# Performance work log

Measured on AMD Instinct MI355X. Metric: run time of the kernel, lower is better.

## Reference

```python
import jax, jax.numpy as jnp
import numpy as np

B, F0, D = 4096, 39, 16
CROSS_LAYER_SIZE = (128, 128)


def _he_uniform(key, shape):
    fan_in = int(np.prod(shape[:-1]))
    limit = np.sqrt(6.0 / fan_in)
    return jax.random.uniform(key, shape, jnp.float32, -limit, limit)


def setup_inputs() -> dict:
    key = jax.random.key(0)
    k_x, k_f0, k_f1, k_w, k_b = jax.random.split(key, 5)
    x = jax.random.normal(k_x, (B, F0, D), dtype=jnp.float32)
    # field_nums with direct=False: [39, 128//2=64, 64]
    f0 = _he_uniform(k_f0, (F0 * F0, CROSS_LAYER_SIZE[0]))          # (1521, 128)
    f1 = _he_uniform(k_f1, (F0 * (CROSS_LAYER_SIZE[0] // 2), CROSS_LAYER_SIZE[1]))  # (2496, 128)
    out_dim = CROSS_LAYER_SIZE[0] // 2 + CROSS_LAYER_SIZE[1]        # 192
    dense_w = _he_uniform(k_w, (out_dim, 1))
    dense_b = jnp.zeros((1,), dtype=jnp.float32)
    return {"x": x, "f0": f0, "f1": f1, "dense_w": dense_w, "dense_b": dense_b}


def reference(x, f0, f1, dense_w, dense_b):
    # CIN forward (direct=False, use_bias=False, use_residual=False, relu)
    # x: (B, F0, D)
    filters = [f0, f1]
    n_layers = len(CROSS_LAYER_SIZE)
    h = x  # hidden state, (B, Fk, D)
    finals = []
    for idx, L in enumerate(CROSS_LAYER_SIZE):
        Fk = h.shape[1]
        # filter f_ has shape (F0*Fk, L) with i (field of x0) major, j (field of h) minor
        Wr = filters[idx].reshape(F0, Fk, L)
        # fused outer product + conv1d (kernel width 1 == matmul over i,j):
        # z[b, m, d] = sum_{i,j} x[b,i,d] * h[b,j,d] * W[i,j,m]
        z = jnp.einsum('bid,bjd,ijm->bmd', x, h, Wr)  # (B, L, D)
        z = jax.nn.relu(z)
        if idx != n_layers - 1:
            # split along feature-map axis: first half feeds next layer,
            # second half goes to output
            h = z[:, : L // 2, :]
            finals.append(z[:, L // 2:, :])
        else:
            finals.append(z)
    result = jnp.sum(jnp.concatenate(finals, axis=1), axis=-1)  # (B, 192)
    return result @ dense_w + dense_b  # (B, 1)
```

## Files before the change

### kernel.cpp

```cpp
#include <hip/hip_runtime.h>


typedef _Float16 h2    __attribute__((ext_vector_type(2)));
typedef _Float16 f16x8 __attribute__((ext_vector_type(8)));
typedef __attribute__((ext_vector_type(16))) float f32x16;

#define XBB 1160
#define L0C 30
#define NCH 110

__device__ __constant__ int IG0[L0C] = {0,0,0,0,0, 1,1,1,1,1, 2,2,2,2, 3,3,3,3, 4,4,4, 5,5,5, 6,6, 7,7, 8, 9};
__device__ __constant__ int JG0[L0C] = {0,1,2,3,4, 0,1,2,3,4, 1,2,3,4, 1,2,3,4, 2,3,4, 2,3,4, 3,4, 3,4, 4, 4};
#define IG0T(c) ((c)<5?0:(c)<10?1:(c)<14?2:(c)<18?3:(c)<21?4:(c)<24?5:(c)<26?6:(c)<28?7:(c)<29?8:9)
#define JG0T(c) ((c)<10?((c)%5):(c)<18?(((c)-10)%4+1):(c)<24?(((c)-18)%3+2):(c)<28?(((c)-24)%2+3):4)

__global__ __launch_bounds__(256)
void CIN_repack(const float* __restrict__ f0, const float* __restrict__ f1,
                uint4* __restrict__ ws)
{
    const int tid  = blockIdx.x * 256 + threadIdx.x;
    const int n    = tid & 127;
    const int slot = tid >> 7;
    const int half = slot & 1;
    const int kh   = (slot >> 1) & 1;
    const int ch   = slot >> 2;
    float v[8];
    if (ch < L0C) {
        const int ig = IG0[ch], jg = JG0[ch];
        const int i = ig * 4 + kh * 2 + half;
#pragma unroll
        for (int t = 0; t < 8; ++t) {
            const int j = jg * 8 + t;
            float val = 0.f;
            if (i < 39 && j < 39 && j >= i) {
                val = f0[(i * 39 + j) * 128 + n];
                if (j > i) val += f0[(j * 39 + i) * 128 + n];
            }
            v[t] = val;
        }
    } else {
        const int c1 = ch - L0C;
        const int jg = c1 / 5, ig = c1 - jg * 5;
        const int j = jg * 4 + kh * 2 + half;
#pragma unroll
        for (int t = 0; t < 8; ++t) {
            const int i = ig * 8 + t;
            v[t] = (i < 39) ? f1[(i * 64 + j) * 128 + n] : 0.f;
        }
    }
    union { h2 h[4]; uint4 q; } pk;
#pragma unroll
    for (int t = 0; t < 4; ++t)
        pk.h[t] = h2{(_Float16)v[2 * t], (_Float16)v[2 * t + 1]};
    const int lane = half * 32 + (n & 31);
    const int cg   = n >> 5;
    ws[ch * 512 + kh * 256 + cg * 64 + lane] = pk.q;
}

__global__ __launch_bounds__(256, 2)
void CIN_main(const float* __restrict__ x,
              const char* __restrict__ wsB,
              const float* __restrict__ dw,
              const float* __restrict__ db,
              float* __restrict__ out)
{
    __shared__ __align__(16) _Float16 xsH[8 * XBB];
    __shared__ __align__(4)  _Float16 hsH[8][64][18];
    __shared__ float dws[192];
    __shared__ float red[4][4];

    const int tid  = threadIdx.x;
    const int w    = tid >> 6;
    const int wp   = w >> 1;
    const int wn   = w & 1;
    const int lane = tid & 63;
    const int half = lane >> 5;
    const int d    = lane & 15;
    const int bsel = (lane >> 4) & 1;
    const int col  = lane & 31;

    const char* wbase = wsB + lane * 16 + wn * 2048 + 2560;
    f16x8 Bb[2][2][2];
    auto loadBg = [&](int ch, f16x8 (&B)[2][2]) {
        const char* p0 = wbase + (size_t)ch * 8192;
        B[0][0] = *(const f16x8*)(p0 - 2560);
        B[0][1] = *(const f16x8*)(p0 - 1536);
        B[1][0] = *(const f16x8*)(p0 + 1536);
        B[1][1] = *(const f16x8*)(p0 + 2560);
    };

    loadBg(0, Bb[0]);
    loadBg(1, Bb[1]);

    const float4* xg4 = (const float4*)(x + (size_t)blockIdx.x * 8 * 624);
    for (int e4 = tid; e4 < 1248; e4 += 256) {
        float4 v = xg4[e4];
        int bb = e4 / 156, r = e4 - bb * 156;
        int i = r >> 2, d0 = (r & 3) * 4;
        _Float16* bp = xsH + bb * XBB + i;
        bp[(d0 + 0) * 72] = (_Float16)v.x; bp[(d0 + 1) * 72] = (_Float16)v.y;
        bp[(d0 + 2) * 72] = (_Float16)v.z; bp[(d0 + 3) * 72] = (_Float16)v.w;
    }
    if (tid < 128) { int bb = tid >> 4, dd = tid & 15; xsH[bb * XBB + dd * 72 + 39] = (_Float16)0.f; }
    if (tid < 192) dws[tid] = dw[tid];
    __syncthreads();

    const _Float16* xrow[2] = {
        xsH + ((wp * 2 + 0) * 2 + bsel) * XBB + d * 72,
        xsH + ((wp * 2 + 1) * 2 + bsel) * XBB + d * 72
    };

    h2 xw[2][20];
#pragma unroll
    for (int p = 0; p < 2; ++p)
#pragma unroll
        for (int w5 = 0; w5 < 5; ++w5) {
            union { f16x8 v; h2 h[4]; } u;
            u.v = *(const f16x8*)(xrow[p] + w5 * 8);
#pragma unroll
            for (int q = 0; q < 4; ++q) xw[p][w5 * 4 + q] = u.h[q];
        }

    f32x16 acc[2][2];
#pragma unroll
    for (int p = 0; p < 2; ++p)
#pragma unroll
        for (int nq = 0; nq < 2; ++nq)
#pragma unroll
            for (int r = 0; r < 16; ++r) acc[p][nq][r] = 0.f;

    h2 sp2[2][2];

#pragma unroll
    for (int c = 0; c < L0C; ++c) {
        const int ig = IG0T(c);
        const int jg = JG0T(c);
        if ((c == 0) || (IG0T(c) != IG0T(c - 1))) {
#pragma unroll
            for (int p = 0; p < 2; ++p)
#pragma unroll
                for (int kh = 0; kh < 2; ++kh) {
                    const h2 pr = xw[p][ig * 2 + kh];
                    const _Float16 vv = half ? pr.y : pr.x;
                    sp2[p][kh] = h2{vv, vv};
                }
        }
#pragma unroll
        for (int p = 0; p < 2; ++p) {
            union { h2 h[4]; f16x8 v; } a0, a1;
#pragma unroll
            for (int q = 0; q < 4; ++q) {
                a0.h[q] = sp2[p][0] * xw[p][jg * 4 + q];
                a1.h[q] = sp2[p][1] * xw[p][jg * 4 + q];
            }
            acc[p][0] = __builtin_amdgcn_mfma_f32_32x32x16_f16(a0.v, Bb[c & 1][0][0], acc[p][0], 0, 0, 0);
            acc[p][1] = __builtin_amdgcn_mfma_f32_32x32x16_f16(a0.v, Bb[c & 1][0][1], acc[p][1], 0, 0, 0);
            acc[p][0] = __builtin_amdgcn_mfma_f32_32x32x16_f16(a1.v, Bb[c & 1][1][0], acc[p][0], 0, 0, 0);
            acc[p][1] = __builtin_amdgcn_mfma_f32_32x32x16_f16(a1.v, Bb[c & 1][1][1], acc[p][1], 0, 0, 0);
        }
        loadBg(c + 2, Bb[c & 1]);
        __builtin_amdgcn_s_barrier();
    }

    float cs[4] = {0.f, 0.f, 0.f, 0.f};
    if (wn == 0) {
#pragma unroll
        for (int p = 0; p < 2; ++p)
#pragma unroll
            for (int nq = 0; nq < 2; ++nq)
#pragma unroll
                for (int r = 0; r < 16; r += 2) {
                    const int row = (r & 3) + 8 * (r >> 2) + 4 * half;
                    h2 pr = h2{(_Float16)fmaxf(acc[p][nq][r],     0.f),
                               (_Float16)fmaxf(acc[p][nq][r + 1], 0.f)};
                    *(h2*)&hsH[(wp * 2 + p) * 2 + (row >> 4)][nq * 32 + col][row & 15] = pr;
                }
    } else {
#pragma unroll
        for (int nq = 0; nq < 2; ++nq) {
            const float dwv = dws[nq * 32 + col];
#pragma unroll
            for (int p = 0; p < 2; ++p)
#pragma unroll
                for (int r = 0; r < 16; ++r) {
                    const int row = (r & 3) + 8 * (r >> 2) + 4 * half;
                    cs[p * 2 + (row >> 4)] += fmaxf(acc[p][nq][r], 0.f) * dwv;
                }
        }
    }
#pragma unroll
    for (int p = 0; p < 2; ++p)
#pragma unroll
        for (int nq = 0; nq < 2; ++nq)
#pragma unroll
            for (int r = 0; r < 16; ++r) acc[p][nq][r] = 0.f;
    __syncthreads();

#pragma unroll 1
    for (int o2 = 0; o2 < 4; ++o2) {
#pragma unroll
        for (int u = 0; u < 20; ++u) {
            const int ig2 = u % 5;
            if (ig2 == 0) {
                const int jb = (o2 * 4 + u / 5) * 4;
#pragma unroll
                for (int p = 0; p < 2; ++p)
#pragma unroll
                    for (int kh = 0; kh < 2; ++kh) {
                        const _Float16 s = hsH[(wp * 2 + p) * 2 + bsel][jb + kh * 2 + half][d];
                        sp2[p][kh] = h2{s, s};
                    }
            }
#pragma unroll
            for (int p = 0; p < 2; ++p) {
                union { h2 h[4]; f16x8 v; } a0, a1;
#pragma unroll
                for (int q = 0; q < 4; ++q) {
                    a0.h[q] = sp2[p][0] * xw[p][ig2 * 4 + q];
                    a1.h[q] = sp2[p][1] * xw[p][ig2 * 4 + q];
                }
                acc[p][0] = __builtin_amdgcn_mfma_f32_32x32x16_f16(a0.v, Bb[u & 1][0][0], acc[p][0], 0, 0, 0);
                acc[p][1] = __builtin_amdgcn_mfma_f32_32x32x16_f16(a0.v, Bb[u & 1][0][1], acc[p][1], 0, 0, 0);
                acc[p][0] = __builtin_amdgcn_mfma_f32_32x32x16_f16(a1.v, Bb[u & 1][1][0], acc[p][0], 0, 0, 0);
                acc[p][1] = __builtin_amdgcn_mfma_f32_32x32x16_f16(a1.v, Bb[u & 1][1][1], acc[p][1], 0, 0, 0);
            }
            int chn = 30 + o2 * 20 + u + 2; if (chn > NCH - 1) chn = NCH - 1;
            loadBg(chn, Bb[u & 1]);
            __builtin_amdgcn_s_barrier();
        }
    }

#pragma unroll
    for (int nq = 0; nq < 2; ++nq) {
        const float dwv = dws[64 + (wn * 2 + nq) * 32 + col];
#pragma unroll
        for (int p = 0; p < 2; ++p)
#pragma unroll
            for (int r = 0; r < 16; ++r) {
                const int row = (r & 3) + 8 * (r >> 2) + 4 * half;
                cs[p * 2 + (row >> 4)] += fmaxf(acc[p][nq][r], 0.f) * dwv;
            }
    }
#pragma unroll
    for (int rr = 0; rr < 4; ++rr)
#pragma unroll
        for (int off = 32; off > 0; off >>= 1)
            cs[rr] += __shfl_xor(cs[rr], off, 64);
    if (lane == 0) {
#pragma unroll
        for (int rr = 0; rr < 4; ++rr) red[w][rr] = cs[rr];
    }
    __syncthreads();
    if (tid < 8) {
        const int wpp = tid >> 2, l = tid & 3;
        out[blockIdx.x * 8 + tid] = red[wpp * 2][l] + red[wpp * 2 + 1][l] + db[0];
    }
}

extern "C" void kernel_launch(void* const* d_in, const int* in_sizes, int n_in,
                              void* d_out, int out_size, void* d_ws, size_t ws_size,
                              hipStream_t stream)
{
    const float* x  = (const float*)d_in[0];
    const float* f0 = (const float*)d_in[1];
    const float* f1 = (const float*)d_in[2];
    const float* dw = (const float*)d_in[3];
    const float* db = (const float*)d_in[4];
    float* out = (float*)d_out;

    CIN_repack<<<dim3(220), dim3(256), 0, stream>>>(f0, f1, (uint4*)d_ws);
    CIN_main<<<dim3(512), dim3(256), 0, stream>>>(x, (const char*)d_ws, dw, db, out);
}
```

Measured before the change: 118.5 us.

## Stage filter chunks through LDS with direct global-to-LDS loads, 4-deep ring

Filter chunks are no longer loaded from global memory into per-wave registers. Each wave now copies a quarter of every chunk into a 4-slot shared-memory ring using global_load_lds, and all waves read their B fragments from LDS. A vmcnt wait plus a workgroup barrier at the top of each step keeps the ring consistent. This halves redundant global traffic, since both wn waves previously fetched overlapping data, and frees the double-buffered B registers. In exchange it adds 32KB of LDS, which may lower occupancy below two blocks per CU, and adds LDS reads inside the MFMA loop.

```diff
diff --git a/kernel.cpp b/kernel.cpp
--- a/kernel.cpp
+++ b/kernel.cpp
@@ -64,6 +64,7 @@
               const float* __restrict__ db,
               float* __restrict__ out)
 {
+    __shared__ __align__(16) char bBc[4 * 8192];
     __shared__ __align__(16) _Float16 xsH[8 * XBB];
     __shared__ __align__(4)  _Float16 hsH[8][64][18];
     __shared__ float dws[192];
@@ -79,18 +80,19 @@
     const int bsel = (lane >> 4) & 1;
     const int col  = lane & 31;
 
-    const char* wbase = wsB + lane * 16 + wn * 2048 + 2560;
-    f16x8 Bb[2][2][2];
-    auto loadBg = [&](int ch, f16x8 (&B)[2][2]) {
-        const char* p0 = wbase + (size_t)ch * 8192;
-        B[0][0] = *(const f16x8*)(p0 - 2560);
-        B[0][1] = *(const f16x8*)(p0 - 1536);
-        B[1][0] = *(const f16x8*)(p0 + 1536);
-        B[1][1] = *(const f16x8*)(p0 + 2560);
+    auto stageB = [&](int ch, int buf) {
+        const char* src = wsB + (size_t)ch * 8192 + w * 2048 + lane * 16;
+        char* dst = bBc + buf * 8192 + w * 2048;
+        __builtin_amdgcn_global_load_lds(
+            (const __attribute__((address_space(1))) void*)(src),
+            (__attribute__((address_space(3))) void*)(dst), 16, 0, 0);
+        __builtin_amdgcn_global_load_lds(
+            (const __attribute__((address_space(1))) void*)(src + 1024),
+            (__attribute__((address_space(3))) void*)(dst + 1024), 16, 0, 0);
     };
 
-    loadBg(0, Bb[0]);
-    loadBg(1, Bb[1]);
+    stageB(0, 0);
+    stageB(1, 1);
 
     const float4* xg4 = (const float4*)(x + (size_t)blockIdx.x * 8 * 624);
     for (int e4 = tid; e4 < 1248; e4 += 256) {
@@ -130,9 +132,13 @@
             for (int r = 0; r < 16; ++r) acc[p][nq][r] = 0.f;
 
     h2 sp2[2][2];
+    const char* bfr = bBc + wn * 2048 + (size_t)lane * 16;
 
 #pragma unroll
     for (int c = 0; c < L0C; ++c) {
+        asm volatile("s_waitcnt vmcnt(2)" ::: "memory");
+        __builtin_amdgcn_sched_barrier(0);
+        __builtin_amdgcn_s_barrier();
         const int ig = IG0T(c);
         const int jg = JG0T(c);
         if ((c == 0) || (IG0T(c) != IG0T(c - 1))) {
@@ -145,6 +151,12 @@
                     sp2[p][kh] = h2{vv, vv};
                 }
         }
+        const char* bb = bfr + (c & 3) * 8192;
+        const f16x8 B00 = *(const f16x8*)(bb);
+        const f16x8 B01 = *(const f16x8*)(bb + 1024);
+        const f16x8 B10 = *(const f16x8*)(bb + 4096);
+        const f16x8 B11 = *(const f16x8*)(bb + 5120);
+        stageB(c + 2, (c + 2) & 3);
 #pragma unroll
         for (int p = 0; p < 2; ++p) {
             union { h2 h[4]; f16x8 v; } a0, a1;
@@ -153,13 +165,11 @@
                 a0.h[q] = sp2[p][0] * xw[p][jg * 4 + q];
                 a1.h[q] = sp2[p][1] * xw[p][jg * 4 + q];
             }
-            acc[p][0] = __builtin_amdgcn_mfma_f32_32x32x16_f16(a0.v, Bb[c & 1][0][0], acc[p][0], 0, 0, 0);
-            acc[p][1] = __builtin_amdgcn_mfma_f32_32x32x16_f16(a0.v, Bb[c & 1][0][1], acc[p][1], 0, 0, 0);
-            acc[p][0] = __builtin_amdgcn_mfma_f32_32x32x16_f16(a1.v, Bb[c & 1][1][0], acc[p][0], 0, 0, 0);
-            acc[p][1] = __builtin_amdgcn_mfma_f32_32x32x16_f16(a1.v, Bb[c & 1][1][1], acc[p][1], 0, 0, 0);
-        }
-        loadBg(c + 2, Bb[c & 1]);
-        __builtin_amdgcn_s_barrier();
+            acc[p][0] = __builtin_amdgcn_mfma_f32_32x32x16_f16(a0.v, B00, acc[p][0], 0, 0, 0);
+            acc[p][1] = __builtin_amdgcn_mfma_f32_32x32x16_f16(a0.v, B01, acc[p][1], 0, 0, 0);
+            acc[p][0] = __builtin_amdgcn_mfma_f32_32x32x16_f16(a1.v, B10, acc[p][0], 0, 0, 0);
+            acc[p][1] = __builtin_amdgcn_mfma_f32_32x32x16_f16(a1.v, B11, acc[p][1], 0, 0, 0);
+        }
     }
 
     float cs[4] = {0.f, 0.f, 0.f, 0.f};
@@ -200,6 +210,9 @@
     for (int o2 = 0; o2 < 4; ++o2) {
 #pragma unroll
         for (int u = 0; u < 20; ++u) {
+            asm volatile("s_waitcnt vmcnt(2)" ::: "memory");
+            __builtin_amdgcn_sched_barrier(0);
+            __builtin_amdgcn_s_barrier();
             const int ig2 = u % 5;
             if (ig2 == 0) {
                 const int jb = (o2 * 4 + u / 5) * 4;
@@ -211,6 +224,13 @@
                         sp2[p][kh] = h2{s, s};
                     }
             }
+            const char* bb = bfr + ((2 + u) & 3) * 8192;
+            const f16x8 B00 = *(const f16x8*)(bb);
+            const f16x8 B01 = *(const f16x8*)(bb + 1024);
+            const f16x8 B10 = *(const f16x8*)(bb + 4096);
+            const f16x8 B11 = *(const f16x8*)(bb + 5120);
+            int chn = 30 + o2 * 20 + u + 2; if (chn > NCH - 1) chn = NCH - 1;
+            stageB(chn, u & 3);
 #pragma unroll
             for (int p = 0; p < 2; ++p) {
                 union { h2 h[4]; f16x8 v; } a0, a1;
@@ -219,14 +239,11 @@
                     a0.h[q] = sp2[p][0] * xw[p][ig2 * 4 + q];
                     a1.h[q] = sp2[p][1] * xw[p][ig2 * 4 + q];
                 }
-                acc[p][0] = __builtin_amdgcn_mfma_f32_32x32x16_f16(a0.v, Bb[u & 1][0][0], acc[p][0], 0, 0, 0);
-                acc[p][1] = __builtin_amdgcn_mfma_f32_32x32x16_f16(a0.v, Bb[u & 1][0][1], acc[p][1], 0, 0, 0);
-                acc[p][0] = __builtin_amdgcn_mfma_f32_32x32x16_f16(a1.v, Bb[u & 1][1][0], acc[p][0], 0, 0, 0);
-                acc[p][1] = __builtin_amdgcn_mfma_f32_32x32x16_f16(a1.v, Bb[u & 1][1][1], acc[p][1], 0, 0, 0);
-            }
-            int chn = 30 + o2 * 20 + u + 2; if (chn > NCH - 1) chn = NCH - 1;
-            loadBg(chn, Bb[u & 1]);
-            __builtin_amdgcn_s_barrier();
+                acc[p][0] = __builtin_amdgcn_mfma_f32_32x32x16_f16(a0.v, B00, acc[p][0], 0, 0, 0);
+                acc[p][1] = __builtin_amdgcn_mfma_f32_32x32x16_f16(a0.v, B01, acc[p][1], 0, 0, 0);
+                acc[p][0] = __builtin_amdgcn_mfma_f32_32x32x16_f16(a1.v, B10, acc[p][0], 0, 0, 0);
+                acc[p][1] = __builtin_amdgcn_mfma_f32_32x32x16_f16(a1.v, B11, acc[p][1], 0, 0, 0);
+            }
         }
     }
 
```

Result: no change. 120.3 us (+1.5%).
